# Performance work log

Hardware: AMD Instinct MI355X
Metric: run time of the kernel (lower is better)

## Reference

```python
import jax, jax.numpy as jnp
import numpy as np

N_NODES = 100000
N_EDGES = 1600000
D_IN = 128
D_HID = 128


def setup_inputs() -> dict:
    key = jax.random.key(0)
    ks = jax.random.split(key, 7)
    s_in = 1.0 / np.sqrt(D_IN)
    s_hid = 1.0 / np.sqrt(D_HID)
    return {
        "x": jax.random.normal(ks[0], (N_NODES, D_IN), dtype=jnp.float32),
        "edge_index": jax.random.randint(ks[1], (2, N_EDGES), 0, N_NODES, dtype=jnp.int64),
        "W1_l": jax.random.normal(ks[2], (D_IN, D_HID), dtype=jnp.float32) * s_in,
        "b1": jnp.zeros((D_HID,), dtype=jnp.float32),
        "W1_r": jax.random.normal(ks[3], (D_IN, D_HID), dtype=jnp.float32) * s_in,
        "W2_l": jax.random.normal(ks[4], (D_HID, D_HID), dtype=jnp.float32) * s_hid,
        "b2": jnp.zeros((D_HID,), dtype=jnp.float32),
        "W2_r": jax.random.normal(ks[5], (D_HID, D_HID), dtype=jnp.float32) * s_hid,
    }


def _mean_aggregate(x, src, dst, num_nodes):
    # messages x[src] mean-aggregated at dst (PyG SAGEConv default aggr='mean')
    msg = jnp.take(x, src, axis=0)                       # [E, D] gather
    summed = jax.ops.segment_sum(msg, dst, num_segments=num_nodes)  # [N, D]
    deg = jax.ops.segment_sum(jnp.ones((src.shape[0],), x.dtype), dst,
                              num_segments=num_nodes)
    return summed / jnp.maximum(deg, 1.0)[:, None]


def _sage_conv(x, src, dst, W_l, b, W_r):
    agg = _mean_aggregate(x, src, dst, x.shape[0])
    # out = lin_l(aggregated neighbors) + lin_r(root)
    return agg @ W_l + b + x @ W_r


def reference(x, edge_index, W1_l, b1, W1_r, W2_l, b2, W2_r):
    src, dst = edge_index[0], edge_index[1]
    h = _sage_conv(x, src, dst, W1_l, b1, W1_r)
    h = jax.nn.relu(h)  # dropout inactive in eval mode
    out = _sage_conv(h, src, dst, W2_l, b2, W2_r)
    return out
```

## Files before the change

### kernel.cpp

```cpp
#include <hip/hip_runtime.h>

#define NN 100000
#define NE 1600000
#define DF 128
#define NBUCK 391
#define PA_BLOCKS 784
#define PB_BLOCKS 391
#define CX_BLOCKS 3125
#define CW_BLOCKS 64
#define AGG_GRID 1568

typedef short short8 __attribute__((ext_vector_type(8)));
typedef float floatx4 __attribute__((ext_vector_type(4)));
typedef float floatx2 __attribute__((ext_vector_type(2)));
typedef unsigned int uintx4 __attribute__((ext_vector_type(4)));
typedef unsigned int uint;
typedef unsigned short ushort;
typedef unsigned char uchar;

static __device__ __forceinline__ ushort f2bf(float f) {
    uint u = __builtin_bit_cast(uint, f);
    return (ushort)((u + 0x7fffu + ((u >> 16) & 1u)) >> 16);
}

__global__ __launch_bounds__(256) void pA_hist(const int* __restrict__ dst,
                                               int* __restrict__ gcnt) {
    __shared__ int h[NBUCK];
    int tid = threadIdx.x;
    for (int i = tid; i < NBUCK; i += 256) h[i] = 0;
    __syncthreads();
    int eb = blockIdx.x * 2048 + tid;
    #pragma unroll
    for (int k = 0; k < 8; ++k) {
        int e = eb + k * 256;
        if (e < NE) atomicAdd(&h[dst[e] >> 8], 1);
    }
    __syncthreads();
    for (int i = tid; i < NBUCK; i += 256)
        if (h[i]) atomicAdd(&gcnt[i], h[i]);
}

__global__ __launch_bounds__(512) void pS_scan(const int* __restrict__ gcnt,
                                               int* __restrict__ goff,
                                               int* __restrict__ gcur) {
    __shared__ int s[512];
    int tid = threadIdx.x;
    int v = (tid < NBUCK) ? gcnt[tid] : 0;
    s[tid] = v;
    __syncthreads();
    for (int st = 1; st < 512; st <<= 1) {
        int t = (tid >= st) ? s[tid - st] : 0;
        __syncthreads();
        s[tid] += t;
        __syncthreads();
    }
    if (tid < NBUCK) {
        int e = s[tid] - v;
        goff[tid] = e;
        gcur[tid] = e;
    }
    if (tid == 0) goff[NBUCK] = NE;
}

__global__ __launch_bounds__(512) void fused_mid(
        const int* __restrict__ src, const int* __restrict__ dst,
        int* __restrict__ gcur, uint2* __restrict__ pairs,
        const float* __restrict__ x, ushort* __restrict__ xb, uint* __restrict__ xf8c,
        const float* __restrict__ W1l, const float* __restrict__ W1r,
        const float* __restrict__ W2l, const float* __restrict__ W2r,
        ushort* __restrict__ WT1, ushort* __restrict__ WT2) {
    __shared__ int h[NBUCK];
    __shared__ int base[NBUCK];
    int bid = blockIdx.x;
    int tid = threadIdx.x;
    if (bid < PB_BLOCKS) {
        for (int i = tid; i < NBUCK; i += 512) h[i] = 0;
        __syncthreads();
        int eb = bid * 4096 + tid;
        int bkt[8], dv[8];
        #pragma unroll
        for (int k = 0; k < 8; ++k) {
            int e = eb + k * 512;
            bkt[k] = -1;
            if (e < NE) {
                int d = dst[e];
                dv[k] = d;
                bkt[k] = d >> 8;
                atomicAdd(&h[bkt[k]], 1);
            }
        }
        __syncthreads();
        for (int i = tid; i < NBUCK; i += 512) {
            base[i] = h[i] ? atomicAdd(&gcur[i], h[i]) : 0;
            h[i] = 0;
        }
        __syncthreads();
        #pragma unroll
        for (int k = 0; k < 8; ++k) {
            int e = eb + k * 512;
            if (e < NE) {
                int r = atomicAdd(&h[bkt[k]], 1);
                pairs[base[bkt[k]] + r] = make_uint2((uint)src[e], (uint)dv[k]);
            }
        }
    } else if (bid < PB_BLOCKS + CX_BLOCKS) {
        int j = (bid - PB_BLOCKS) * 512 + tid;
        int p = j / (NN * 4);
        int rem = j - p * (NN * 4);
        int node = rem >> 2, q2 = rem & 3;
        const float4* xr = (const float4*)(x + (size_t)node * 128 + p * 32 + q2 * 8);
        float4 v0 = xr[0], v1 = xr[1];
        uint4 ob;
        ob.x = (uint)f2bf(v0.x) | ((uint)f2bf(v0.y) << 16);
        ob.y = (uint)f2bf(v0.z) | ((uint)f2bf(v0.w) << 16);
        ob.z = (uint)f2bf(v1.x) | ((uint)f2bf(v1.y) << 16);
        ob.w = (uint)f2bf(v1.z) | ((uint)f2bf(v1.w) << 16);
        *(uint4*)(xb + (size_t)node * 128 + p * 32 + q2 * 8) = ob;
        uint pk0 = (uint)__builtin_amdgcn_cvt_pk_fp8_f32(v0.x, v0.y, 0, false);
        pk0 = (uint)__builtin_amdgcn_cvt_pk_fp8_f32(v0.z, v0.w, (int)pk0, true);
        uint pk1 = (uint)__builtin_amdgcn_cvt_pk_fp8_f32(v1.x, v1.y, 0, false);
        pk1 = (uint)__builtin_amdgcn_cvt_pk_fp8_f32(v1.z, v1.w, (int)pk1, true);
        ((uint2*)xf8c)[j] = make_uint2(pk0, pk1);
    } else {
        int id = (bid - PB_BLOCKS - CX_BLOCKS) * 512 + tid;
        int n = id >> 8, k = id & 255;
        float a = (k < 128) ? W1l[k * 128 + n] : W1r[(k - 128) * 128 + n];
        float b = (k < 128) ? W2l[k * 128 + n] : W2r[(k - 128) * 128 + n];
        WT1[id] = f2bf(a);
        WT2[id] = f2bf(b);
    }
}

__global__ __launch_bounds__(256) void pC_scatter(const uint2* __restrict__ pairs,
                                                  const int* __restrict__ goff,
                                                  int* __restrict__ off,
                                                  int* __restrict__ srt) {
    __shared__ int deg[256];
    __shared__ int loc[256];
    int b = blockIdx.x;
    int beg = goff[b], end = goff[b + 1];
    int tid = threadIdx.x;
    deg[tid] = 0;
    __syncthreads();
    for (int i = beg + tid; i < end; i += 256)
        atomicAdd(&deg[pairs[i].y & 255], 1);
    __syncthreads();
    int v = deg[tid];
    loc[tid] = v;
    __syncthreads();
    for (int st = 1; st < 256; st <<= 1) {
        int t = (tid >= st) ? loc[tid - st] : 0;
        __syncthreads();
        loc[tid] += t;
        __syncthreads();
    }
    int excl = loc[tid] - v + beg;
    int n = (b << 8) + tid;
    if (n < NN) off[n] = excl;
    __syncthreads();
    deg[tid] = excl;
    __syncthreads();
    for (int i = beg + tid; i < end; i += 256) {
        uint2 pr = pairs[i];
        int pos = atomicAdd(&deg[pr.y & 255], 1);
        srt[pos] = (int)pr.x;
    }
}

static __device__ __forceinline__ void acc8(floatx2* ac, uint2 v) {
    ac[0] += __builtin_amdgcn_cvt_pk_f32_fp8((int)v.x, false);
    ac[1] += __builtin_amdgcn_cvt_pk_f32_fp8((int)v.x, true);
    ac[2] += __builtin_amdgcn_cvt_pk_f32_fp8((int)v.y, false);
    ac[3] += __builtin_amdgcn_cvt_pk_f32_fp8((int)v.y, true);
}

#define AGG_LOOP(IDX)                                            \
    {                                                            \
        int i = lb;                                              \
        for (; i + 8 <= le; i += 8) {                            \
            int idx[8];                                          \
            _Pragma("unroll")                                    \
            for (int k = 0; k < 8; ++k) idx[k] = IDX(i + k);     \
            uint2 v[8];                                          \
            _Pragma("unroll")                                    \
            for (int k = 0; k < 8; ++k) v[k] = f[(size_t)idx[k] * 4]; \
            _Pragma("unroll")                                    \
            for (int k = 0; k < 8; ++k) acc8(ac, v[k]);          \
        }                                                        \
        if (i + 4 <= le) {                                       \
            int idx[4];                                          \
            _Pragma("unroll")                                    \
            for (int k = 0; k < 4; ++k) idx[k] = IDX(i + k);     \
            uint2 v[4];                                          \
            _Pragma("unroll")                                    \
            for (int k = 0; k < 4; ++k) v[k] = f[(size_t)idx[k] * 4]; \
            _Pragma("unroll")                                    \
            for (int k = 0; k < 4; ++k) acc8(ac, v[k]);          \
            i += 4;                                              \
        }                                                        \
        for (; i < le; ++i) {                                    \
            uint2 v = f[(size_t)IDX(i) * 4];                     \
            acc8(ac, v);                                         \
        }                                                        \
    }

__global__ __launch_bounds__(256) void agg_csr(const uint* __restrict__ feat8,
                                               const int* __restrict__ srt,
                                               const int* __restrict__ off,
                                               ushort* __restrict__ aggb) {
    __shared__ int sidx[2048];
    int bid = blockIdx.x;
    int p = bid / AGG_GRID;
    int nb = (bid - p * AGG_GRID) * 64;
    if (nb >= NN) return;
    int tid = threadIdx.x;

    int segb = off[nb];
    int nend = nb + 64;
    int sege = (nend < NN) ? off[nend] : NE;
    int stage = min(sege - segb, 2048);
    for (int i = tid; i < stage; i += 256) sidx[i] = srt[segb + i];
    __syncthreads();

    int n = nb + (tid >> 2);
    int l = tid & 3;
    if (n >= NN) return;
    const uint2* f = (const uint2*)(feat8 + (size_t)p * (NN * 8)) + l;

    int beg = off[n];
    int end = (n < NN - 1) ? off[n + 1] : NE;
    int lb = beg - segb, le = end - segb;

    floatx2 ac[4];
    #pragma unroll
    for (int t = 0; t < 4; ++t) ac[t] = (floatx2){0.f, 0.f};

    if (le <= stage) {
        #define IDX_LDS(ii) sidx[ii]
        AGG_LOOP(IDX_LDS)
        #undef IDX_LDS
    } else {
        #define IDX_GBL(ii) srt[segb + (ii)]
        AGG_LOOP(IDX_GBL)
        #undef IDX_GBL
    }

    float inv = 1.0f / fmaxf((float)(end - beg), 1.0f);
    uintx4 o;
    o.x = (uint)f2bf(ac[0].x * inv) | ((uint)f2bf(ac[0].y * inv) << 16);
    o.y = (uint)f2bf(ac[1].x * inv) | ((uint)f2bf(ac[1].y * inv) << 16);
    o.z = (uint)f2bf(ac[2].x * inv) | ((uint)f2bf(ac[2].y * inv) << 16);
    o.w = (uint)f2bf(ac[3].x * inv) | ((uint)f2bf(ac[3].y * inv) << 16);
    uintx4* dp = (uintx4*)(aggb + (size_t)n * 128 + p * 32 + l * 8);
    __builtin_nontemporal_store(o, dp);
}

template <int RELU, int BF16OUT, int F8OUT>
__global__ __launch_bounds__(512, 4) void gemm_mfma(
        const ushort* __restrict__ aggb, const ushort* __restrict__ selfb,
        const ushort* __restrict__ WT, const float* __restrict__ bias,
        void* __restrict__ outv, uchar* __restrict__ f8out) {
    __shared__ ushort sWT[128 * 256];
    const int tid = threadIdx.x;
    const int blk = blockIdx.x;

    #pragma unroll
    for (int it = 0; it < 8; ++it) {
        int flat = it * 512 + tid;
        int col = flat >> 5;
        int c = flat & 31;
        uint4 v = *(const uint4*)(WT + (size_t)col * 256 + c * 8);
        *(uint4*)&sWT[col * 256 + (c ^ (col & 7)) * 8] = v;
    }

    const int w = tid >> 6;
    const int lane = tid & 63;
    const int m = lane & 15;
    const int q = lane >> 4;

    int node_m = blk * 128 + w * 16 + m;
    int cn = node_m < NN ? node_m : NN - 1;
    const ushort* arow = aggb + (size_t)cn * 128;
    const ushort* xrow = selfb + (size_t)cn * 128;
    short8 a[8];
    #pragma unroll
    for (int kk = 0; kk < 4; ++kk) {
        a[kk]     = *(const short8*)(arow + kk * 32 + q * 8);
        a[4 + kk] = *(const short8*)(xrow + kk * 32 + q * 8);
    }

    __syncthreads();

    floatx4 acc[8];
    #pragma unroll
    for (int t = 0; t < 8; ++t) acc[t] = (floatx4){0.f, 0.f, 0.f, 0.f};

    const int m7 = m & 7;
    #pragma unroll
    for (int kk = 0; kk < 8; ++kk) {
        int cx = (kk * 4 + q) ^ m7;
        #pragma unroll
        for (int t = 0; t < 8; ++t) {
            short8 b = *(const short8*)&sWT[(t * 16 + m) * 256 + cx * 8];
            acc[t] = __builtin_amdgcn_mfma_f32_16x16x32_bf16(a[kk], b, acc[t], 0, 0, 0);
        }
    }

    const int node_base = blk * 128 + w * 16 + q * 4;
    #pragma unroll
    for (int t = 0; t < 8; ++t) {
        int col = t * 16 + m;
        float bj = bias[col];
        #pragma unroll
        for (int r = 0; r < 4; ++r) {
            int node = node_base + r;
            if (node < NN) {
                float v = acc[t][r] + bj;
                if (RELU) v = fmaxf(v, 0.0f);
                if (BF16OUT)
                    ((ushort*)outv)[(size_t)node * 128 + col] = f2bf(v);
                else
                    ((float*)outv)[(size_t)node * 128 + col] = v;
                if (F8OUT) {
                    uint pk = (uint)__builtin_amdgcn_cvt_pk_fp8_f32(v, v, 0, false);
                    f8out[((size_t)(col >> 5) * NN + node) * 32 + (col & 31)] =
                        (uchar)pk;
                }
            }
        }
    }
}

extern "C" void kernel_launch(void* const* d_in, const int* in_sizes, int n_in,
                              void* d_out, int out_size, void* d_ws, size_t ws_size,
                              hipStream_t stream) {
    const float* x   = (const float*)d_in[0];
    const int*   ei  = (const int*)d_in[1];
    const float* W1l = (const float*)d_in[2];
    const float* b1  = (const float*)d_in[3];
    const float* W1r = (const float*)d_in[4];
    const float* W2l = (const float*)d_in[5];
    const float* b2  = (const float*)d_in[6];
    const float* W2r = (const float*)d_in[7];
    float*       out = (float*)d_out;

    const int* src = ei;
    const int* dst = ei + NE;

    char* ws = (char*)d_ws;
    int*    off  = (int*)(ws);
    int*    srt  = (int*)(ws + 400000);
    ushort* WT1  = (ushort*)(ws + 7200000);
    ushort* WT2  = (ushort*)(ws + 7265536);
    ushort* xb   = (ushort*)(ws + 7331072);
    uint*   xf8c = (uint*)(ws + 32931072);
    ushort* aggb = (ushort*)(ws + 45731072);
    ushort* hb   = (ushort*)(ws + 71331072);
    uchar*  hf8c = (uchar*)xf8c;
    uint2*  pairs = (uint2*)aggb;
    int*    gcnt  = (int*)((char*)aggb + 12800000);
    int*    goff  = (int*)((char*)aggb + 12801600);
    int*    gcur  = (int*)((char*)aggb + 12803200);

    (void)hipMemsetAsync(gcnt, 0, NBUCK * 4, stream);
    pA_hist<<<PA_BLOCKS, 256, 0, stream>>>(dst, gcnt);
    pS_scan<<<1, 512, 0, stream>>>(gcnt, goff, gcur);
    fused_mid<<<PB_BLOCKS + CX_BLOCKS + CW_BLOCKS, 512, 0, stream>>>(
        src, dst, gcur, pairs, x, xb, xf8c, W1l, W1r, W2l, W2r, WT1, WT2);
    pC_scatter<<<NBUCK, 256, 0, stream>>>(pairs, goff, off, srt);

    const int gemm_grid = (NN + 127) / 128;

    agg_csr<<<4 * AGG_GRID, 256, 0, stream>>>(xf8c, srt, off, aggb);
    gemm_mfma<1, 1, 1><<<gemm_grid, 512, 0, stream>>>(aggb, xb, WT1, b1, hb, hf8c);

    agg_csr<<<4 * AGG_GRID, 256, 0, stream>>>((const uint*)hf8c, srt, off, aggb);
    gemm_mfma<0, 0, 0><<<gemm_grid, 512, 0, stream>>>(aggb, hb, WT2, b2, out, nullptr);
}
```

Measured before the change: 223.8 us.

## Switch fp8 feature table to row-major and gather 16 bytes per lane

Replaces the column-chunked fp8 feature layout (four 32-byte slices per node in separate planes) with a plain row-major 128-byte row per node. The aggregation kernel now has 8 lanes each loading 16 bytes per neighbor, covering the full row in one pass instead of launching four passes over the edge list. This removes the repeated reading of CSR indices and offsets for each feature chunk, and each gather fetches a full 128-byte line. In exchange each block covers 32 nodes instead of 64 with more registers per thread, and the GEMM's fp8 output writes become single-byte stores strided across rows.

Measured after the change: 195.2 us. 1.15x faster.

```diff
diff --git a/kernel.cpp b/kernel.cpp
--- a/kernel.cpp
+++ b/kernel.cpp
@@ -8,7 +8,7 @@
 #define PB_BLOCKS 391
 #define CX_BLOCKS 3125
 #define CW_BLOCKS 64
-#define AGG_GRID 1568
+#define AGG_GRID 3128
 
 typedef short short8 __attribute__((ext_vector_type(8)));
 typedef float floatx4 __attribute__((ext_vector_type(4)));
@@ -65,7 +65,7 @@
 __global__ __launch_bounds__(512) void fused_mid(
         const int* __restrict__ src, const int* __restrict__ dst,
         int* __restrict__ gcur, uint2* __restrict__ pairs,
-        const float* __restrict__ x, ushort* __restrict__ xb, uint* __restrict__ xf8c,
+        const float* __restrict__ x, ushort* __restrict__ xb, uint* __restrict__ xf8,
         const float* __restrict__ W1l, const float* __restrict__ W1r,
         const float* __restrict__ W2l, const float* __restrict__ W2r,
         ushort* __restrict__ WT1, ushort* __restrict__ WT2) {
@@ -105,22 +105,19 @@
         }
     } else if (bid < PB_BLOCKS + CX_BLOCKS) {
         int j = (bid - PB_BLOCKS) * 512 + tid;
-        int p = j / (NN * 4);
-        int rem = j - p * (NN * 4);
-        int node = rem >> 2, q2 = rem & 3;
-        const float4* xr = (const float4*)(x + (size_t)node * 128 + p * 32 + q2 * 8);
+        const float4* xr = (const float4*)x + (size_t)j * 2;
         float4 v0 = xr[0], v1 = xr[1];
         uint4 ob;
         ob.x = (uint)f2bf(v0.x) | ((uint)f2bf(v0.y) << 16);
         ob.y = (uint)f2bf(v0.z) | ((uint)f2bf(v0.w) << 16);
         ob.z = (uint)f2bf(v1.x) | ((uint)f2bf(v1.y) << 16);
         ob.w = (uint)f2bf(v1.z) | ((uint)f2bf(v1.w) << 16);
-        *(uint4*)(xb + (size_t)node * 128 + p * 32 + q2 * 8) = ob;
+        ((uint4*)xb)[j] = ob;
         uint pk0 = (uint)__builtin_amdgcn_cvt_pk_fp8_f32(v0.x, v0.y, 0, false);
         pk0 = (uint)__builtin_amdgcn_cvt_pk_fp8_f32(v0.z, v0.w, (int)pk0, true);
         uint pk1 = (uint)__builtin_amdgcn_cvt_pk_fp8_f32(v1.x, v1.y, 0, false);
         pk1 = (uint)__builtin_amdgcn_cvt_pk_fp8_f32(v1.z, v1.w, (int)pk1, true);
-        ((uint2*)xf8c)[j] = make_uint2(pk0, pk1);
+        ((uint2*)xf8)[j] = make_uint2(pk0, pk1);
     } else {
         int id = (bid - PB_BLOCKS - CX_BLOCKS) * 512 + tid;
         int n = id >> 8, k = id & 255;
@@ -167,11 +164,15 @@
     }
 }
 
-static __device__ __forceinline__ void acc8(floatx2* ac, uint2 v) {
+static __device__ __forceinline__ void acc16(floatx2* ac, uint4 v) {
     ac[0] += __builtin_amdgcn_cvt_pk_f32_fp8((int)v.x, false);
     ac[1] += __builtin_amdgcn_cvt_pk_f32_fp8((int)v.x, true);
     ac[2] += __builtin_amdgcn_cvt_pk_f32_fp8((int)v.y, false);
     ac[3] += __builtin_amdgcn_cvt_pk_f32_fp8((int)v.y, true);
+    ac[4] += __builtin_amdgcn_cvt_pk_f32_fp8((int)v.z, false);
+    ac[5] += __builtin_amdgcn_cvt_pk_f32_fp8((int)v.z, true);
+    ac[6] += __builtin_amdgcn_cvt_pk_f32_fp8((int)v.w, false);
+    ac[7] += __builtin_amdgcn_cvt_pk_f32_fp8((int)v.w, true);
 }
 
 #define AGG_LOOP(IDX)                                            \
@@ -181,26 +182,26 @@
             int idx[8];                                          \
             _Pragma("unroll")                                    \
             for (int k = 0; k < 8; ++k) idx[k] = IDX(i + k);     \
-            uint2 v[8];                                          \
-            _Pragma("unroll")                                    \
-            for (int k = 0; k < 8; ++k) v[k] = f[(size_t)idx[k] * 4]; \
-            _Pragma("unroll")                                    \
-            for (int k = 0; k < 8; ++k) acc8(ac, v[k]);          \
+            uint4 v[8];                                          \
+            _Pragma("unroll")                                    \
+            for (int k = 0; k < 8; ++k) v[k] = f[(size_t)idx[k] * 8]; \
+            _Pragma("unroll")                                    \
+            for (int k = 0; k < 8; ++k) acc16(ac, v[k]);         \
         }                                                        \
         if (i + 4 <= le) {                                       \
             int idx[4];                                          \
             _Pragma("unroll")                                    \
             for (int k = 0; k < 4; ++k) idx[k] = IDX(i + k);     \
-            uint2 v[4];                                          \
-            _Pragma("unroll")                                    \
-            for (int k = 0; k < 4; ++k) v[k] = f[(size_t)idx[k] * 4]; \
-            _Pragma("unroll")                                    \
-            for (int k = 0; k < 4; ++k) acc8(ac, v[k]);          \
+            uint4 v[4];                                          \
+            _Pragma("unroll")                                    \
+            for (int k = 0; k < 4; ++k) v[k] = f[(size_t)idx[k] * 8]; \
+            _Pragma("unroll")                                    \
+            for (int k = 0; k < 4; ++k) acc16(ac, v[k]);         \
             i += 4;                                              \
         }                                                        \
         for (; i < le; ++i) {                                    \
-            uint2 v = f[(size_t)IDX(i) * 4];                     \
-            acc8(ac, v);                                         \
+            uint4 v = f[(size_t)IDX(i) * 8];                     \
+            acc16(ac, v);                                        \
         }                                                        \
     }
 
@@ -209,31 +210,29 @@
                                                const int* __restrict__ off,
                                                ushort* __restrict__ aggb) {
     __shared__ int sidx[2048];
-    int bid = blockIdx.x;
-    int p = bid / AGG_GRID;
-    int nb = (bid - p * AGG_GRID) * 64;
+    int nb = blockIdx.x * 32;
     if (nb >= NN) return;
     int tid = threadIdx.x;
 
     int segb = off[nb];
-    int nend = nb + 64;
+    int nend = nb + 32;
     int sege = (nend < NN) ? off[nend] : NE;
     int stage = min(sege - segb, 2048);
     for (int i = tid; i < stage; i += 256) sidx[i] = srt[segb + i];
     __syncthreads();
 
-    int n = nb + (tid >> 2);
-    int l = tid & 3;
+    int n = nb + (tid >> 3);
+    int l = tid & 7;
     if (n >= NN) return;
-    const uint2* f = (const uint2*)(feat8 + (size_t)p * (NN * 8)) + l;
+    const uint4* f = (const uint4*)feat8 + l;
 
     int beg = off[n];
     int end = (n < NN - 1) ? off[n + 1] : NE;
     int lb = beg - segb, le = end - segb;
 
-    floatx2 ac[4];
-    #pragma unroll
-    for (int t = 0; t < 4; ++t) ac[t] = (floatx2){0.f, 0.f};
+    floatx2 ac[8];
+    #pragma unroll
+    for (int t = 0; t < 8; ++t) ac[t] = (floatx2){0.f, 0.f};
 
     if (le <= stage) {
         #define IDX_LDS(ii) sidx[ii]
@@ -246,13 +245,18 @@
     }
 
     float inv = 1.0f / fmaxf((float)(end - beg), 1.0f);
-    uintx4 o;
-    o.x = (uint)f2bf(ac[0].x * inv) | ((uint)f2bf(ac[0].y * inv) << 16);
-    o.y = (uint)f2bf(ac[1].x * inv) | ((uint)f2bf(ac[1].y * inv) << 16);
-    o.z = (uint)f2bf(ac[2].x * inv) | ((uint)f2bf(ac[2].y * inv) << 16);
-    o.w = (uint)f2bf(ac[3].x * inv) | ((uint)f2bf(ac[3].y * inv) << 16);
-    uintx4* dp = (uintx4*)(aggb + (size_t)n * 128 + p * 32 + l * 8);
-    __builtin_nontemporal_store(o, dp);
+    uintx4 o0, o1;
+    o0.x = (uint)f2bf(ac[0].x * inv) | ((uint)f2bf(ac[0].y * inv) << 16);
+    o0.y = (uint)f2bf(ac[1].x * inv) | ((uint)f2bf(ac[1].y * inv) << 16);
+    o0.z = (uint)f2bf(ac[2].x * inv) | ((uint)f2bf(ac[2].y * inv) << 16);
+    o0.w = (uint)f2bf(ac[3].x * inv) | ((uint)f2bf(ac[3].y * inv) << 16);
+    o1.x = (uint)f2bf(ac[4].x * inv) | ((uint)f2bf(ac[4].y * inv) << 16);
+    o1.y = (uint)f2bf(ac[5].x * inv) | ((uint)f2bf(ac[5].y * inv) << 16);
+    o1.z = (uint)f2bf(ac[6].x * inv) | ((uint)f2bf(ac[6].y * inv) << 16);
+    o1.w = (uint)f2bf(ac[7].x * inv) | ((uint)f2bf(ac[7].y * inv) << 16);
+    uintx4* dp = (uintx4*)(aggb + (size_t)n * 128 + l * 16);
+    __builtin_nontemporal_store(o0, dp);
+    __builtin_nontemporal_store(o1, dp + 1);
 }
 
 template <int RELU, int BF16OUT, int F8OUT>
@@ -323,8 +327,7 @@
                     ((float*)outv)[(size_t)node * 128 + col] = v;
                 if (F8OUT) {
                     uint pk = (uint)__builtin_amdgcn_cvt_pk_fp8_f32(v, v, 0, false);
-                    f8out[((size_t)(col >> 5) * NN + node) * 32 + (col & 31)] =
-                        (uchar)pk;
+                    f8out[(size_t)node * 128 + col] = (uchar)pk;
                 }
             }
         }
@@ -353,10 +356,10 @@
     ushort* WT1  = (ushort*)(ws + 7200000);
     ushort* WT2  = (ushort*)(ws + 7265536);
     ushort* xb   = (ushort*)(ws + 7331072);
-    uint*   xf8c = (uint*)(ws + 32931072);
+    uint*   xf8  = (uint*)(ws + 32931072);
     ushort* aggb = (ushort*)(ws + 45731072);
     ushort* hb   = (ushort*)(ws + 71331072);
-    uchar*  hf8c = (uchar*)xf8c;
+    uchar*  hf8  = (uchar*)xf8;
     uint2*  pairs = (uint2*)aggb;
     int*    gcnt  = (int*)((char*)aggb + 12800000);
     int*    goff  = (int*)((char*)aggb + 12801600);
@@ -366,14 +369,14 @@
     pA_hist<<<PA_BLOCKS, 256, 0, stream>>>(dst, gcnt);
     pS_scan<<<1, 512, 0, stream>>>(gcnt, goff, gcur);
     fused_mid<<<PB_BLOCKS + CX_BLOCKS + CW_BLOCKS, 512, 0, stream>>>(
-        src, dst, gcur, pairs, x, xb, xf8c, W1l, W1r, W2l, W2r, WT1, WT2);
+        src, dst, gcur, pairs, x, xb, xf8, W1l, W1r, W2l, W2r, WT1, WT2);
     pC_scatter<<<NBUCK, 256, 0, stream>>>(pairs, goff, off, srt);
 
     const int gemm_grid = (NN + 127) / 128;
 
-    agg_csr<<<4 * AGG_GRID, 256, 0, stream>>>(xf8c, srt, off, aggb);
-    gemm_mfma<1, 1, 1><<<gemm_grid, 512, 0, stream>>>(aggb, xb, WT1, b1, hb, hf8c);
-
-    agg_csr<<<4 * AGG_GRID, 256, 0, stream>>>((const uint*)hf8c, srt, off, aggb);
+    agg_csr<<<AGG_GRID, 256, 0, stream>>>(xf8, srt, off, aggb);
+    gemm_mfma<1, 1, 1><<<gemm_grid, 512, 0, stream>>>(aggb, xb, WT1, b1, hb, hf8);
+
+    agg_csr<<<AGG_GRID, 256, 0, stream>>>((const uint*)hf8, srt, off, aggb);
     gemm_mfma<0, 0, 0><<<gemm_grid, 512, 0, stream>>>(aggb, hb, WT2, b2, out, nullptr);
 }
```
